# Kernel tuning notes

Hardware: AMD Instinct MI355X
Metric: run time of the kernel (lower is better)

## Reference

```python
import jax, jax.numpy as jnp
import numpy as np

# Model dims (eval mode: dropout off, no gate noise, no KV cache, start_pos=0)
B, T, C = 2, 2048, 1024
H, KV = 16, 4
HD = C // H            # 64
E, K = 8, 2            # n_experts, active_experts
FE, FS = 1024, 2048    # expert_inter_dim, shared inter_dim
EPS = 1e-6
BASE = 10000.0


def setup_inputs() -> dict:
    key = jax.random.key(0)
    ks = jax.random.split(key, 15)
    s = 0.02
    f32 = jnp.float32
    return {
        'x': jax.random.normal(ks[0], (B, T, C), f32),
        'norm1_w': jnp.ones((C,), f32),
        'norm2_w': jnp.ones((C,), f32),
        'wq': jax.random.normal(ks[1], (C, H * HD), f32) * s,
        'wk': jax.random.normal(ks[2], (C, KV * HD), f32) * s,
        'wv': jax.random.normal(ks[3], (C, KV * HD), f32) * s,
        'wo': jax.random.normal(ks[4], (H * HD, C), f32) * s,
        'gate_w': jax.random.normal(ks[5], (C, E), f32) * s,
        'exp_w1': jax.random.normal(ks[6], (E, C, FE), f32) * s,
        'exp_w2': jax.random.normal(ks[7], (E, C, FE), f32) * s,
        'exp_wp': jax.random.normal(ks[8], (E, FE, C), f32) * s,
        'sh_w1': jax.random.normal(ks[9], (C, FS), f32) * s,
        'sh_w2': jax.random.normal(ks[10], (C, FS), f32) * s,
        'sh_wp': jax.random.normal(ks[11], (FS, C), f32) * s,
    }


def _rms(x, w):
    return x * jax.lax.rsqrt(jnp.mean(x * x, -1, keepdims=True) + EPS) * w


def _rope_table(t, hd):
    freqs = 1.0 / (BASE ** (jnp.arange(0, hd, 2, dtype=jnp.float32) / hd))
    ang = jnp.outer(jnp.arange(t, dtype=jnp.float32), freqs)  # (T, hd/2)
    return jnp.stack([jnp.cos(ang), jnp.sin(ang)], -1)        # (T, hd/2, 2)


def _apply_rope(x, fc):
    # x: (B, T, nH, hd); fc: (T, hd/2, 2)
    xr = x.reshape(*x.shape[:-1], -1, 2)
    cos = fc[None, :, None, :, 0]
    sin = fc[None, :, None, :, 1]
    out = jnp.stack([xr[..., 0] * cos - xr[..., 1] * sin,
                     xr[..., 1] * cos + xr[..., 0] * sin], -1)
    return out.reshape(x.shape).astype(x.dtype)


def reference(x, norm1_w, norm2_w, wq, wk, wv, wo, gate_w,
              exp_w1, exp_w2, exp_wp, sh_w1, sh_w2, sh_wp):
    fc = _rope_table(T, HD)
    # --- GQA attention with RoPE ---
    h1 = _rms(x, norm1_w)
    q = (h1 @ wq).reshape(B, T, H, HD)
    k = (h1 @ wk).reshape(B, T, KV, HD)
    v = (h1 @ wv).reshape(B, T, KV, HD)
    q = _apply_rope(q, fc)
    k = _apply_rope(k, fc)
    rep = H // KV
    k = jnp.repeat(k, rep, axis=2)  # (B,T,H,HD)
    v = jnp.repeat(v, rep, axis=2)
    scores = jnp.einsum('bqhd,bkhd->bhqk', q, k) / jnp.sqrt(jnp.float32(HD))
    mask = jnp.where(jnp.tril(jnp.ones((T, T), bool)), 0.0, -1e9).astype(scores.dtype)
    att = jax.nn.softmax(scores + mask, axis=-1)
    o = jnp.einsum('bhqk,bkhd->bqhd', att, v).reshape(B, T, C) @ wo
    x1 = x + o
    # --- MoE block (top-k gate, dense masked combine == gather/scatter math) ---
    h2 = _rms(x1, norm2_w).reshape(-1, C)  # (N, C), N = B*T
    gate_logits = h2 @ gate_w              # (N, E)
    p = jax.nn.softmax(gate_logits, axis=-1)
    topw, topi = jax.lax.top_k(p, K)       # values == gather(p, indices)
    comb = jnp.sum(jax.nn.one_hot(topi, E, dtype=p.dtype) * topw[..., None], axis=1)  # (N, E)
    he = jax.nn.silu(jnp.einsum('nc,ecf->enf', h2, exp_w1)) * jnp.einsum('nc,ecf->enf', h2, exp_w2)
    ye = jnp.einsum('enf,efc->enc', he, exp_wp)
    y = jnp.einsum('enc,ne->nc', ye, comb)
    z = (jax.nn.silu(h2 @ sh_w1) * (h2 @ sh_w2)) @ sh_wp
    out = x1 + (y + z).reshape(B, T, C)
    return out, gate_logits
```

## Files before the change

kernel.cpp:

```cpp
#include <hip/hip_runtime.h>
#include <hip/hip_bf16.h>

#define TB 2
#define TT 2048
#define TC 1024
#define TH 16
#define TKV 4
#define THD 64
#define TE 8
#define TFE 1024
#define TFS 2048
#define NTOK 4096
#define NSLOT 8192

typedef __attribute__((ext_vector_type(4))) float f32x4;
typedef __attribute__((ext_vector_type(16))) float f32x16;
typedef __attribute__((ext_vector_type(8))) short s16x8;

__device__ __forceinline__ float bf2f(short s) {
    unsigned int u = ((unsigned int)(unsigned short)s) << 16;
    return __builtin_bit_cast(float, u);
}
__device__ __forceinline__ short f2bf(float f) {
    unsigned int u = __builtin_bit_cast(unsigned int, f);
    u = u + 0x7fffu + ((u >> 16) & 1u);
    return (short)(u >> 16);
}
__device__ __forceinline__ unsigned int cvtpk_bf16(float lo, float hi) {
    unsigned int r;
    asm volatile("v_cvt_pk_bf16_f32 %0, %1, %2" : "=v"(r) : "v"(lo), "v"(hi));
    return r;
}

__device__ __forceinline__ void gl_lds16(const void* g, void* l) {
    __builtin_amdgcn_global_load_lds((const __attribute__((address_space(1))) void*)g,
                                     (__attribute__((address_space(3))) void*)l,
                                     16, 0, 0);
}

__global__ __launch_bounds__(256) void k_transp(const float* __restrict__ in,
                                                short* __restrict__ out,
                                                int R, int Cd,
                                                size_t bs_in, size_t bs_out) {
    __shared__ float tile[32][33];
    const float* ip = in + bs_in * blockIdx.z;
    short* op = out + bs_out * blockIdx.z;
    int tx = threadIdx.x & 31, ty = threadIdx.x >> 5;
    int r0 = blockIdx.y * 32, c0 = blockIdx.x * 32;
    #pragma unroll
    for (int r = ty; r < 32; r += 8)
        tile[r][tx] = ip[(size_t)(r0 + r) * Cd + c0 + tx];
    __syncthreads();
    #pragma unroll
    for (int r = ty; r < 32; r += 8)
        op[(size_t)(c0 + r) * R + r0 + tx] = f2bf(tile[tx][r]);
}

__global__ __launch_bounds__(256) void k_transp_v(const short* __restrict__ qkv,
                                                  short* __restrict__ v_t) {
    __shared__ short tile[32][33];
    int z = blockIdx.z;
    int b = z >> 2, kvh = z & 3;
    const short* ip = qkv + (size_t)b * TT * 1536 + 1280 + kvh * 64;
    short* op = v_t + (size_t)z * THD * TT;
    int tx = threadIdx.x & 31, ty = threadIdx.x >> 5;
    int t0 = blockIdx.y * 32, d0 = blockIdx.x * 32;
    #pragma unroll
    for (int r = ty; r < 32; r += 8)
        tile[r][tx] = ip[(size_t)(t0 + r) * 1536 + d0 + tx];
    __syncthreads();
    #pragma unroll
    for (int r = ty; r < 32; r += 8)
        op[(size_t)(d0 + r) * TT + t0 + tx] = tile[tx][r];
}

__global__ void k_rope_table(float* __restrict__ rope) {
    int idx = blockIdx.x * 256 + threadIdx.x;
    if (idx >= TT * 32) return;
    int t = idx >> 5, i = idx & 31;
    float freq = expf(-(float)i * (1.0f / 32.0f) * 9.210340371976184f);
    float ang = (float)t * freq;
    rope[idx * 2 + 0] = cosf(ang);
    rope[idx * 2 + 1] = sinf(ang);
}

__global__ __launch_bounds__(256) void k_rmsnorm(const float* __restrict__ x,
                                                 const float* __restrict__ w,
                                                 short* __restrict__ out) {
    int row = blockIdx.x, t = threadIdx.x;
    float4 v = ((const float4*)(x + (size_t)row * TC))[t];
    float ss = v.x * v.x + v.y * v.y + v.z * v.z + v.w * v.w;
    #pragma unroll
    for (int off = 32; off; off >>= 1) ss += __shfl_xor(ss, off);
    __shared__ float red[4];
    if ((t & 63) == 0) red[t >> 6] = ss;
    __syncthreads();
    float rs = rsqrtf((red[0] + red[1] + red[2] + red[3]) * (1.0f / 1024.0f) + 1e-6f);
    float4 wv = ((const float4*)w)[t];
    short4 o;
    o.x = f2bf(v.x * rs * wv.x);
    o.y = f2bf(v.y * rs * wv.y);
    o.z = f2bf(v.z * rs * wv.z);
    o.w = f2bf(v.w * rs * wv.w);
    ((short4*)(out + (size_t)row * TC))[t] = o;
}

template <int EPI>
__global__ __launch_bounds__(256) void k_gemm128(const short* __restrict__ A,
                                                 const short* __restrict__ Bt,
                                                 void* __restrict__ outp,
                                                 const float* __restrict__ resid,
                                                 int M, int N, int K) {
    __shared__ short As0[128 * 32], As1[128 * 32];
    __shared__ short Bs0[128 * 32], Bs1[128 * 32];
    int tid = threadIdx.x;
    int brow = blockIdx.y * 128, bcol = blockIdx.x * 128;
    int wid = tid >> 6, lane = tid & 63;
    int wr = wid >> 1, wc = wid & 1, g = lane >> 4, c = lane & 15;
    int srow = wid * 32 + (lane >> 2);
    int scol = (lane & 3) * 8;
    const short* Ag0 = A + (size_t)(brow + srow) * K + scol;
    const short* Ag1 = A + (size_t)(brow + srow + 16) * K + scol;
    const short* Bg0 = Bt + (size_t)(bcol + srow) * K + scol;
    const short* Bg1 = Bt + (size_t)(bcol + srow + 16) * K + scol;
    int loff = __builtin_amdgcn_readfirstlane(wid * 2048);
    f32x4 acc[4][4] = {};

    gl_lds16(Ag0, (char*)As0 + loff);
    gl_lds16(Ag1, (char*)As0 + loff + 1024);
    gl_lds16(Bg0, (char*)Bs0 + loff);
    gl_lds16(Bg1, (char*)Bs0 + loff + 1024);
    __syncthreads();

    short* Ac = As0; short* Bc = Bs0;
    short* Aa = As1; short* Ba = Bs1;
    for (int kk = 0; kk < K; kk += 32) {
        int kn = kk + 32;
        if (kn < K) {
            gl_lds16(Ag0 + kn, (char*)Aa + loff);
            gl_lds16(Ag1 + kn, (char*)Aa + loff + 1024);
            gl_lds16(Bg0 + kn, (char*)Ba + loff);
            gl_lds16(Bg1 + kn, (char*)Ba + loff + 1024);
        }
        s16x8 af[4], bf[4];
        #pragma unroll
        for (int m = 0; m < 4; m++) af[m] = *(const s16x8*)(Ac + (wr * 64 + m * 16 + c) * 32 + g * 8);
        #pragma unroll
        for (int n = 0; n < 4; n++) bf[n] = *(const s16x8*)(Bc + (wc * 64 + n * 16 + c) * 32 + g * 8);
        #pragma unroll
        for (int m = 0; m < 4; m++)
            #pragma unroll
            for (int n = 0; n < 4; n++)
                acc[m][n] = __builtin_amdgcn_mfma_f32_16x16x32_bf16(af[m], bf[n], acc[m][n], 0, 0, 0);
        __syncthreads();
        short* t;
        t = Ac; Ac = Aa; Aa = t;
        t = Bc; Bc = Ba; Ba = t;
    }
    #pragma unroll
    for (int m = 0; m < 4; m++)
        #pragma unroll
        for (int n = 0; n < 4; n++)
            #pragma unroll
            for (int j = 0; j < 4; j++) {
                int row = brow + wr * 64 + m * 16 + g * 4 + j;
                int col = bcol + wc * 64 + n * 16 + c;
                float v = acc[m][n][j];
                if (EPI == 0)
                    ((short*)outp)[(size_t)row * N + col] = f2bf(v);
                else
                    ((float*)outp)[(size_t)row * N + col] = v + resid[(size_t)row * N + col];
            }
}

template <int EPI>
__global__ __launch_bounds__(256) void k_gemm64(const short* __restrict__ A,
                                                const short* __restrict__ Bt,
                                                void* __restrict__ outp,
                                                const float* __restrict__ resid,
                                                int M, int N, int K) {
    __shared__ short As0[128 * 32], As1[128 * 32];
    __shared__ short Bs0[64 * 32], Bs1[64 * 32];
    int tid = threadIdx.x;
    int brow = blockIdx.y * 128, bcol = blockIdx.x * 64;
    int wid = tid >> 6, lane = tid & 63;
    int wr = wid >> 1, wc = wid & 1, g = lane >> 4, c = lane & 15;
    int srow = wid * 32 + (lane >> 2);
    int scol = (lane & 3) * 8;
    const short* Ag0 = A + (size_t)(brow + srow) * K + scol;
    const short* Ag1 = A + (size_t)(brow + srow + 16) * K + scol;
    int sbrow = wid * 16 + (lane >> 2);
    const short* Bg = Bt + (size_t)(bcol + sbrow) * K + scol;
    int loffA = __builtin_amdgcn_readfirstlane(wid * 2048);
    int loffB = __builtin_amdgcn_readfirstlane(wid * 1024);
    f32x4 acc[4][2] = {};

    gl_lds16(Ag0, (char*)As0 + loffA);
    gl_lds16(Ag1, (char*)As0 + loffA + 1024);
    gl_lds16(Bg, (char*)Bs0 + loffB);
    __syncthreads();

    short* Ac = As0; short* Bc = Bs0;
    short* Aa = As1; short* Ba = Bs1;
    for (int kk = 0; kk < K; kk += 32) {
        int kn = kk + 32;
        if (kn < K) {
            gl_lds16(Ag0 + kn, (char*)Aa + loffA);
            gl_lds16(Ag1 + kn, (char*)Aa + loffA + 1024);
            gl_lds16(Bg + kn, (char*)Ba + loffB);
        }
        s16x8 af[4], bf[2];
        #pragma unroll
        for (int m = 0; m < 4; m++) af[m] = *(const s16x8*)(Ac + (wr * 64 + m * 16 + c) * 32 + g * 8);
        #pragma unroll
        for (int n = 0; n < 2; n++) bf[n] = *(const s16x8*)(Bc + (wc * 32 + n * 16 + c) * 32 + g * 8);
        #pragma unroll
        for (int m = 0; m < 4; m++)
            #pragma unroll
            for (int n = 0; n < 2; n++)
                acc[m][n] = __builtin_amdgcn_mfma_f32_16x16x32_bf16(af[m], bf[n], acc[m][n], 0, 0, 0);
        __syncthreads();
        short* t;
        t = Ac; Ac = Aa; Aa = t;
        t = Bc; Bc = Ba; Ba = t;
    }
    #pragma unroll
    for (int m = 0; m < 4; m++)
        #pragma unroll
        for (int n = 0; n < 2; n++)
            #pragma unroll
            for (int j = 0; j < 4; j++) {
                int row = brow + wr * 64 + m * 16 + g * 4 + j;
                int col = bcol + wc * 32 + n * 16 + c;
                float v = acc[m][n][j];
                if (EPI == 0)
                    ((short*)outp)[(size_t)row * N + col] = f2bf(v);
                else
                    ((float*)outp)[(size_t)row * N + col] = v + resid[(size_t)row * N + col];
            }
}

__global__ void k_rope_apply(const short* __restrict__ qkv,
                             const float* __restrict__ rope,
                             short* __restrict__ q_r,
                             short* __restrict__ k_r) {
    int idx = blockIdx.x * 256 + threadIdx.x;
    if (idx >= NTOK * 640) return;
    int row = idx / 640;
    int p = idx - row * 640;
    int b = row >> 11, t = row & 2047;
    const short* src = qkv + (size_t)row * 1536;
    if (p < 512) {
        int h = p >> 5, i = p & 31;
        float x0 = bf2f(src[h * 64 + 2 * i]);
        float x1 = bf2f(src[h * 64 + 2 * i + 1]);
        float cs = rope[(t * 32 + i) * 2], sn = rope[(t * 32 + i) * 2 + 1];
        size_t o = ((size_t)(b * TH + h) * TT + t) * THD + 2 * i;
        q_r[o]     = f2bf(x0 * cs - x1 * sn);
        q_r[o + 1] = f2bf(x1 * cs + x0 * sn);
    } else {
        int pk = p - 512;
        int kv = pk >> 5, i = pk & 31;
        float x0 = bf2f(src[1024 + kv * 64 + 2 * i]);
        float x1 = bf2f(src[1024 + kv * 64 + 2 * i + 1]);
        float cs = rope[(t * 32 + i) * 2], sn = rope[(t * 32 + i) * 2 + 1];
        size_t o = ((size_t)(b * TKV + kv) * TT + t) * THD + 2 * i;
        k_r[o]     = f2bf(x0 * cs - x1 * sn);
        k_r[o + 1] = f2bf(x1 * cs + x0 * sn);
    }
}

__global__ __launch_bounds__(256) void k_attn(const short* __restrict__ q_r,
                                              const short* __restrict__ k_r,
                                              const short* __restrict__ v_t,
                                              short* __restrict__ attn_o) {
    int w = threadIdx.x >> 6, lane = threadIdx.x & 63;
    int qt = 63 - (blockIdx.x * 4 + w);
    int qbase = qt * 32;
    int bh = blockIdx.y;
    int b = bh >> 4, h = bh & 15, kv = h >> 2;
    int q32 = lane & 31, hi = lane >> 5;

    const short* qp = q_r + ((size_t)(b * TH + h) * TT + qbase) * THD;
    const short* kp = k_r + ((size_t)(b * TKV + kv) * TT) * THD;
    const short* vp = v_t + ((size_t)(b * TKV + kv) * THD) * TT;

    s16x8 qf[4];
    #pragma unroll
    for (int dc = 0; dc < 4; dc++)
        qf[dc] = *(const s16x8*)(qp + q32 * THD + dc * 16 + hi * 8);

    f32x16 ot0 = {}, ot1 = {};
    float mrun = -1e30f, lrun = 0.f;
    int nkt = (qbase + 95) >> 6;

    for (int kt = 0; kt < nkt; kt++) {
        int ktb = kt * 64;
        f32x16 st0 = {}, st1 = {};
        s16x8 kf0[4], kf1[4];
        #pragma unroll
        for (int dc = 0; dc < 4; dc++) {
            kf0[dc] = *(const s16x8*)(kp + (size_t)(ktb + q32) * THD + dc * 16 + hi * 8);
            kf1[dc] = *(const s16x8*)(kp + (size_t)(ktb + 32 + q32) * THD + dc * 16 + hi * 8);
        }
        s16x8 vf[8];
        #pragma unroll
        for (int dt = 0; dt < 2; dt++)
            #pragma unroll
            for (int kc = 0; kc < 4; kc++)
                vf[dt * 4 + kc] = *(const s16x8*)(vp + (size_t)(dt * 32 + q32) * TT + ktb + kc * 16 + hi * 8);

        __builtin_amdgcn_s_setprio(1);
        #pragma unroll
        for (int dc = 0; dc < 4; dc++) {
            st0 = __builtin_amdgcn_mfma_f32_32x32x16_bf16(kf0[dc], qf[dc], st0, 0, 0, 0);
            st1 = __builtin_amdgcn_mfma_f32_32x32x16_bf16(kf1[dc], qf[dc], st1, 0, 0, 0);
        }
        __builtin_amdgcn_s_setprio(0);

        bool domask = (kt == nkt - 1);
        int qabs = qbase + q32;
        #pragma unroll
        for (int r = 0; r < 16; r++) {
            int kploc = (r & 3) + 8 * (r >> 2) + 4 * hi;
            float s0 = st0[r] * 0.125f;
            float s1 = st1[r] * 0.125f;
            if (domask) {
                if (ktb + kploc > qabs) s0 = -1e30f;
                if (ktb + 32 + kploc > qabs) s1 = -1e30f;
            }
            st0[r] = s0; st1[r] = s1;
        }
        float pm = st0[0];
        #pragma unroll
        for (int r = 1; r < 16; r++) pm = fmaxf(pm, st0[r]);
        #pragma unroll
        for (int r = 0; r < 16; r++) pm = fmaxf(pm, st1[r]);
        pm = fmaxf(pm, __shfl_xor(pm, 32));
        float mnew = fmaxf(mrun, pm);
        float al = __expf(mrun - mnew);
        mrun = mnew;
        float rs = 0.f;
        #pragma unroll
        for (int r = 0; r < 16; r++) {
            float e0 = __expf(st0[r] - mnew); st0[r] = e0; rs += e0;
            float e1 = __expf(st1[r] - mnew); st1[r] = e1; rs += e1;
        }
        rs += __shfl_xor(rs, 32);
        lrun = lrun * al + rs;
        #pragma unroll
        for (int r = 0; r < 16; r++) { ot0[r] *= al; ot1[r] *= al; }

        unsigned int w0[8], w1[8];
        #pragma unroll
        for (int j = 0; j < 8; j++) {
            w0[j] = cvtpk_bf16(st0[2 * j], st0[2 * j + 1]);
            w1[j] = cvtpk_bf16(st1[2 * j], st1[2 * j + 1]);
        }
        s16x8 pf[4];
        #pragma unroll
        for (int kc = 0; kc < 4; kc++) {
            unsigned int* ww = (kc < 2) ? w0 : w1;
            int kcl = kc & 1;
            unsigned int x0 = ww[4 * kcl + 0], y0 = ww[4 * kcl + 2];
            unsigned int x1 = ww[4 * kcl + 1], y1 = ww[4 * kcl + 3];
            asm volatile("v_permlane32_swap_b32 %0, %1" : "+v"(x0), "+v"(y0));
            asm volatile("v_permlane32_swap_b32 %0, %1" : "+v"(x1), "+v"(y1));
            unsigned int fr[4] = {x0, x1, y0, y1};
            pf[kc] = __builtin_bit_cast(s16x8, *(ulong2*)fr);
        }
        __builtin_amdgcn_s_setprio(1);
        #pragma unroll
        for (int kc = 0; kc < 4; kc++) {
            ot0 = __builtin_amdgcn_mfma_f32_32x32x16_bf16(vf[kc], pf[kc], ot0, 0, 0, 0);
            ot1 = __builtin_amdgcn_mfma_f32_32x32x16_bf16(vf[4 + kc], pf[kc], ot1, 0, 0, 0);
        }
        __builtin_amdgcn_s_setprio(0);
    }
    float inv = 1.0f / lrun;
    short* orow = attn_o + (size_t)(b * TT + qbase + q32) * TC + h * THD;
    #pragma unroll
    for (int s = 0; s < 4; s++) {
        short4 v0, v1;
        v0.x = f2bf(ot0[4 * s + 0] * inv); v0.y = f2bf(ot0[4 * s + 1] * inv);
        v0.z = f2bf(ot0[4 * s + 2] * inv); v0.w = f2bf(ot0[4 * s + 3] * inv);
        v1.x = f2bf(ot1[4 * s + 0] * inv); v1.y = f2bf(ot1[4 * s + 1] * inv);
        v1.z = f2bf(ot1[4 * s + 2] * inv); v1.w = f2bf(ot1[4 * s + 3] * inv);
        *(short4*)(orow + 8 * s + 4 * hi) = v0;
        *(short4*)(orow + 32 + 8 * s + 4 * hi) = v1;
    }
}

__global__ __launch_bounds__(256) void k_gate(const float* __restrict__ x1,
                                              const float* __restrict__ n2w,
                                              const float* __restrict__ gate_w,
                                              float* __restrict__ gl,
                                              int* __restrict__ cnt,
                                              int* __restrict__ te,
                                              int* __restrict__ tls,
                                              float* __restrict__ tw) {
    int w = threadIdx.x >> 6, lane = threadIdx.x & 63;
    int n = blockIdx.x * 4 + w;
    const float* xp = x1 + (size_t)n * TC;
    float ss = 0.f;
    for (int i = lane; i < TC; i += 64) { float v = xp[i]; ss += v * v; }
    #pragma unroll
    for (int off = 32; off; off >>= 1) ss += __shfl_xor(ss, off);
    float rs = rsqrtf(ss * (1.0f / 1024.0f) + 1e-6f);
    int e = lane & 7, ch = lane >> 3;
    float acc = 0.f;
    for (int i = 0; i < 128; i++) {
        int cc = ch * 128 + i;
        acc += xp[cc] * rs * n2w[cc] * gate_w[(size_t)cc * TE + e];
    }
    acc += __shfl_xor(acc, 8);
    acc += __shfl_xor(acc, 16);
    acc += __shfl_xor(acc, 32);
    float logit = acc;
    if (lane < 8) gl[(size_t)n * TE + lane] = logit;
    float mx = logit;
    mx = fmaxf(mx, __shfl_xor(mx, 1)); mx = fmaxf(mx, __shfl_xor(mx, 2)); mx = fmaxf(mx, __shfl_xor(mx, 4));
    float ex = __expf(logit - mx);
    float sm = ex;
    sm += __shfl_xor(sm, 1); sm += __shfl_xor(sm, 2); sm += __shfl_xor(sm, 4);
    float pp = ex / sm;
    float m1 = pp;
    m1 = fmaxf(m1, __shfl_xor(m1, 1)); m1 = fmaxf(m1, __shfl_xor(m1, 2)); m1 = fmaxf(m1, __shfl_xor(m1, 4));
    int cand = (pp == m1) ? e : 8;
    int e0 = cand;
    e0 = min(e0, __shfl_xor(e0, 1)); e0 = min(e0, __shfl_xor(e0, 2)); e0 = min(e0, __shfl_xor(e0, 4));
    float p2 = (e == e0) ? -1.0f : pp;
    float m2 = p2;
    m2 = fmaxf(m2, __shfl_xor(m2, 1)); m2 = fmaxf(m2, __shfl_xor(m2, 2)); m2 = fmaxf(m2, __shfl_xor(m2, 4));
    int cand2 = (p2 == m2) ? e : 8;
    int e1 = cand2;
    e1 = min(e1, __shfl_xor(e1, 1)); e1 = min(e1, __shfl_xor(e1, 2)); e1 = min(e1, __shfl_xor(e1, 4));
    if (lane == 0) {
        int ls0 = atomicAdd(&cnt[e0], 1);
        int ls1 = atomicAdd(&cnt[e1], 1);
        te[n * 2] = e0; te[n * 2 + 1] = e1;
        tls[n * 2] = ls0; tls[n * 2 + 1] = ls1;
        tw[n * 2] = m1; tw[n * 2 + 1] = m2;
    }
}

__global__ void k_prefix(const int* __restrict__ cnt, int* __restrict__ basep) {
    if (threadIdx.x == 0) {
        int s = 0;
        for (int e = 0; e < TE; e++) { basep[e] = s; s += cnt[e]; }
    }
}

__global__ void k_scatter(const int* __restrict__ te, const int* __restrict__ tls,
                          const float* __restrict__ tw, const int* __restrict__ basep,
                          int* __restrict__ tlist, float* __restrict__ slotw,
                          int* __restrict__ sot) {
    int n = blockIdx.x * 256 + threadIdx.x;
    if (n >= NTOK) return;
    int s0 = basep[te[n * 2]] + tls[n * 2];
    int s1 = basep[te[n * 2 + 1]] + tls[n * 2 + 1];
    tlist[s0] = n; tlist[s1] = n;
    slotw[s0] = tw[n * 2]; slotw[s1] = tw[n * 2 + 1];
    sot[n * 2] = s0; sot[n * 2 + 1] = s1;
}

__global__ __launch_bounds__(512) void k_ffn(const short* __restrict__ A,
                                             const short* __restrict__ eB1,
                                             const short* __restrict__ eB2,
                                             const short* __restrict__ sB1,
                                             const short* __restrict__ sB2,
                                             short* __restrict__ he,
                                             short* __restrict__ shm,
                                             const int* __restrict__ cnt,
                                             const int* __restrict__ basep,
                                             const int* __restrict__ tlist,
                                             const float* __restrict__ slotw) {
    int z = blockIdx.z;
    int moe = (z < 8);
    int nt = blockIdx.x, mt = blockIdx.y;
    int ce = 0, base = 0;
    if (moe) {
        if (nt >= 8) return;
        ce = cnt[z];
        if (mt * 128 >= ce) return;
        base = basep[z];
    }
    __shared__ short As0[128 * 32], As1[128 * 32];
    __shared__ short B1s0[128 * 32], B1s1[128 * 32];
    __shared__ short B2s0[128 * 32], B2s1[128 * 32];
    int tid = threadIdx.x, wid = tid >> 6, lane = tid & 63;
    int wr = wid >> 2, wc = wid & 3, g = lane >> 4, c = lane & 15;
    const int K = TC;
    int srow = wid * 16 + (lane >> 2);
    int scol = (lane & 3) * 8;
    size_t arow;
    if (moe) {
        int l0 = mt * 128 + srow; if (l0 >= ce) l0 = ce - 1;
        arow = (size_t)tlist[base + l0];
    } else {
        arow = (size_t)(mt * 128 + srow);
    }
    const short* Ag = A + arow * (size_t)K + scol;
    const short* B1g;
    const short* B2g;
    if (moe) {
        B1g = eB1 + ((size_t)z * TFE + (size_t)(nt * 128 + srow)) * K + scol;
        B2g = eB2 + ((size_t)z * TFE + (size_t)(nt * 128 + srow)) * K + scol;
    } else {
        B1g = sB1 + (size_t)(nt * 128 + srow) * K + scol;
        B2g = sB2 + (size_t)(nt * 128 + srow) * K + scol;
    }
    int loff = __builtin_amdgcn_readfirstlane(wid * 1024);
    f32x4 a1[4][2] = {}, a2[4][2] = {};

    gl_lds16(Ag, (char*)As0 + loff);
    gl_lds16(B1g, (char*)B1s0 + loff);
    gl_lds16(B2g, (char*)B2s0 + loff);
    __syncthreads();

    short* Ac = As0;  short* B1c = B1s0;  short* B2c = B2s0;
    short* Aa = As1;  short* B1a = B1s1;  short* B2a = B2s1;
    for (int kk = 0; kk < K; kk += 32) {
        int kn = kk + 32;
        if (kn < K) {
            gl_lds16(Ag + kn, (char*)Aa + loff);
            gl_lds16(B1g + kn, (char*)B1a + loff);
            gl_lds16(B2g + kn, (char*)B2a + loff);
        }
        s16x8 af[4], b1[2], b2[2];
        #pragma unroll
        for (int m_ = 0; m_ < 4; m_++) af[m_] = *(const s16x8*)(Ac + (wr * 64 + m_ * 16 + c) * 32 + g * 8);
        #pragma unroll
        for (int n = 0; n < 2; n++) {
            b1[n] = *(const s16x8*)(B1c + (wc * 32 + n * 16 + c) * 32 + g * 8);
            b2[n] = *(const s16x8*)(B2c + (wc * 32 + n * 16 + c) * 32 + g * 8);
        }
        #pragma unroll
        for (int m_ = 0; m_ < 4; m_++)
            #pragma unroll
            for (int n = 0; n < 2; n++) {
                a1[m_][n] = __builtin_amdgcn_mfma_f32_16x16x32_bf16(af[m_], b1[n], a1[m_][n], 0, 0, 0);
                a2[m_][n] = __builtin_amdgcn_mfma_f32_16x16x32_bf16(af[m_], b2[n], a2[m_][n], 0, 0, 0);
            }
        __syncthreads();
        short* t;
        t = Ac; Ac = Aa; Aa = t;
        t = B1c; B1c = B1a; B1a = t;
        t = B2c; B2c = B2a; B2a = t;
    }
    #pragma unroll
    for (int m_ = 0; m_ < 4; m_++)
        #pragma unroll
        for (int n = 0; n < 2; n++)
            #pragma unroll
            for (int j = 0; j < 4; j++) {
                int lrow = mt * 128 + wr * 64 + m_ * 16 + g * 4 + j;
                if (moe && lrow >= ce) continue;
                int col = nt * 128 + wc * 32 + n * 16 + c;
                float g1 = a1[m_][n][j], g2 = a2[m_][n][j];
                float v = g1 / (1.0f + __expf(-g1)) * g2;
                if (moe) {
                    v *= slotw[base + lrow];
                    he[(size_t)(base + lrow) * TFE + col] = f2bf(v);
                } else {
                    shm[(size_t)lrow * TFS + col] = f2bf(v);
                }
            }
}

__global__ __launch_bounds__(256) void k_moe2(const short* __restrict__ he,
                                              const short* __restrict__ Wpt,
                                              short* __restrict__ ye,
                                              const int* __restrict__ cnt,
                                              const int* __restrict__ basep) {
    int e = blockIdx.z;
    int ce = cnt[e];
    int mt = blockIdx.y;
    if (mt * 128 >= ce) return;
    int base = basep[e];
    int nt = blockIdx.x;
    __shared__ short As0[128 * 32], As1[128 * 32];
    __shared__ short Bs0[128 * 32], Bs1[128 * 32];
    int tid = threadIdx.x, wid = tid >> 6, lane = tid & 63;
    int wr = wid >> 1, wc = wid & 1, g = lane >> 4, c = lane & 15;
    int srow = wid * 32 + (lane >> 2);
    int scol = (lane & 3) * 8;
    const short* Ag0 = he + (size_t)(base + mt * 128 + srow) * TFE + scol;
    const short* Ag1 = Ag0 + (size_t)16 * TFE;
    const short* Bg0 = Wpt + ((size_t)e * 1024 + nt * 128 + srow) * TFE + scol;
    const short* Bg1 = Bg0 + (size_t)16 * TFE;
    int loff = __builtin_amdgcn_readfirstlane(wid * 2048);
    f32x4 acc[4][4] = {};

    gl_lds16(Ag0, (char*)As0 + loff);
    gl_lds16(Ag1, (char*)As0 + loff + 1024);
    gl_lds16(Bg0, (char*)Bs0 + loff);
    gl_lds16(Bg1, (char*)Bs0 + loff + 1024);
    __syncthreads();

    short* Ac = As0; short* Bc = Bs0;
    short* Aa = As1; short* Ba = Bs1;
    for (int kk = 0; kk < TFE; kk += 32) {
        int kn = kk + 32;
        if (kn < TFE) {
            gl_lds16(Ag0 + kn, (char*)Aa + loff);
            gl_lds16(Ag1 + kn, (char*)Aa + loff + 1024);
            gl_lds16(Bg0 + kn, (char*)Ba + loff);
            gl_lds16(Bg1 + kn, (char*)Ba + loff + 1024);
        }
        s16x8 af[4], bf[4];
        #pragma unroll
        for (int m = 0; m < 4; m++) af[m] = *(const s16x8*)(Ac + (wr * 64 + m * 16 + c) * 32 + g * 8);
        #pragma unroll
        for (int n = 0; n < 4; n++) bf[n] = *(const s16x8*)(Bc + (wc * 64 + n * 16 + c) * 32 + g * 8);
        #pragma unroll
        for (int m = 0; m < 4; m++)
            #pragma unroll
            for (int n = 0; n < 4; n++)
                acc[m][n] = __builtin_amdgcn_mfma_f32_16x16x32_bf16(af[m], bf[n], acc[m][n], 0, 0, 0);
        __syncthreads();
        short* t;
        t = Ac; Ac = Aa; Aa = t;
        t = Bc; Bc = Ba; Ba = t;
    }
    #pragma unroll
    for (int m = 0; m < 4; m++)
        #pragma unroll
        for (int n = 0; n < 4; n++)
            #pragma unroll
            for (int j = 0; j < 4; j++) {
                int lrow = mt * 128 + wr * 64 + m * 16 + g * 4 + j;
                if (lrow >= ce) continue;
                int col = nt * 128 + wc * 64 + n * 16 + c;
                ye[(size_t)(base + lrow) * TC + col] = f2bf(acc[m][n][j]);
            }
}

__global__ __launch_bounds__(256) void k_final(const short* __restrict__ A,
                                               const short* __restrict__ Bt,
                                               const float* __restrict__ x1,
                                               const short* __restrict__ ye,
                                               const int* __restrict__ sot,
                                               float* __restrict__ outp) {
    __shared__ short As0[128 * 32], As1[128 * 32];
    __shared__ short Bs0[64 * 32], Bs1[64 * 32];
    const int K = TFS;
    int tid = threadIdx.x;
    int brow = blockIdx.y * 128, bcol = blockIdx.x * 64;
    int wid = tid >> 6, lane = tid & 63;
    int wr = wid >> 1, wc = wid & 1, g = lane >> 4, c = lane & 15;
    int srow = wid * 32 + (lane >> 2);
    int scol = (lane & 3) * 8;
    const short* Ag0 = A + (size_t)(brow + srow) * K + scol;
    const short* Ag1 = A + (size_t)(brow + srow + 16) * K + scol;
    int sbrow = wid * 16 + (lane >> 2);
    const short* Bg = Bt + (size_t)(bcol + sbrow) * K + scol;
    int loffA = __builtin_amdgcn_readfirstlane(wid * 2048);
    int loffB = __builtin_amdgcn_readfirstlane(wid * 1024);
    f32x4 acc[4][2] = {};

    gl_lds16(Ag0, (char*)As0 + loffA);
    gl_lds16(Ag1, (char*)As0 + loffA + 1024);
    gl_lds16(Bg, (char*)Bs0 + loffB);
    __syncthreads();

    short* Ac = As0; short* Bc = Bs0;
    short* Aa = As1; short* Ba = Bs1;
    for (int kk = 0; kk < K; kk += 32) {
        int kn = kk + 32;
        if (kn < K) {
            gl_lds16(Ag0 + kn, (char*)Aa + loffA);
            gl_lds16(Ag1 + kn, (char*)Aa + loffA + 1024);
            gl_lds16(Bg + kn, (char*)Ba + loffB);
        }
        s16x8 af[4], bf[2];
        #pragma unroll
        for (int m = 0; m < 4; m++) af[m] = *(const s16x8*)(Ac + (wr * 64 + m * 16 + c) * 32 + g * 8);
        #pragma unroll
        for (int n = 0; n < 2; n++) bf[n] = *(const s16x8*)(Bc + (wc * 32 + n * 16 + c) * 32 + g * 8);
        #pragma unroll
        for (int m = 0; m < 4; m++)
            #pragma unroll
            for (int n = 0; n < 2; n++)
                acc[m][n] = __builtin_amdgcn_mfma_f32_16x16x32_bf16(af[m], bf[n], acc[m][n], 0, 0, 0);
        __syncthreads();
        short* t;
        t = Ac; Ac = Aa; Aa = t;
        t = Bc; Bc = Ba; Ba = t;
    }
    #pragma unroll
    for (int m = 0; m < 4; m++)
        #pragma unroll
        for (int n = 0; n < 2; n++)
            #pragma unroll
            for (int j = 0; j < 4; j++) {
                int row = brow + wr * 64 + m * 16 + g * 4 + j;
                int col = bcol + wc * 32 + n * 16 + c;
                int s0 = sot[row * 2], s1 = sot[row * 2 + 1];
                float v = acc[m][n][j] + x1[(size_t)row * TC + col]
                        + bf2f(ye[(size_t)s0 * TC + col]) + bf2f(ye[(size_t)s1 * TC + col]);
                outp[(size_t)row * TC + col] = v;
            }
}

extern "C" void kernel_launch(void* const* d_in, const int* in_sizes, int n_in,
                              void* d_out, int out_size, void* d_ws, size_t ws_size,
                              hipStream_t stream) {
    const float* x     = (const float*)d_in[0];
    const float* n1w   = (const float*)d_in[1];
    const float* n2w   = (const float*)d_in[2];
    const float* wq    = (const float*)d_in[3];
    const float* wk    = (const float*)d_in[4];
    const float* wv    = (const float*)d_in[5];
    const float* wo    = (const float*)d_in[6];
    const float* gatew = (const float*)d_in[7];
    const float* ew1   = (const float*)d_in[8];
    const float* ew2   = (const float*)d_in[9];
    const float* ewp   = (const float*)d_in[10];
    const float* sw1   = (const float*)d_in[11];
    const float* sw2   = (const float*)d_in[12];
    const float* swp   = (const float*)d_in[13];
    float* outp = (float*)d_out;

    char* p = (char*)d_ws;
    auto alloc = [&](size_t bytes) -> char* {
        char* r = p;
        p += (bytes + 255) & ~(size_t)255;
        return r;
    };
    short* wqkv_t = (short*)alloc(1536 * 1024 * 2);
    short* wo_t   = (short*)alloc(1024 * 1024 * 2);
    short* ew1_t  = (short*)alloc((size_t)8 * 1024 * 1024 * 2);
    short* ew2_t  = (short*)alloc((size_t)8 * 1024 * 1024 * 2);
    short* ewp_t  = (short*)alloc((size_t)8 * 1024 * 1024 * 2);
    short* sw1_t  = (short*)alloc((size_t)2048 * 1024 * 2);
    short* sw2_t  = (short*)alloc((size_t)2048 * 1024 * 2);
    short* swp_t  = (short*)alloc((size_t)1024 * 2048 * 2);
    short* h1     = (short*)alloc((size_t)NTOK * 1024 * 2);
    short* qkv    = (short*)alloc((size_t)NTOK * 1536 * 2);
    short* q_r    = (short*)alloc((size_t)TB * TH * TT * THD * 2);
    short* k_r    = (short*)alloc((size_t)TB * TKV * TT * THD * 2);
    short* v_t    = (short*)alloc((size_t)TB * TKV * THD * TT * 2);
    short* attn_o = (short*)alloc((size_t)NTOK * 1024 * 2);
    float* x1     = (float*)alloc((size_t)NTOK * 1024 * 4);
    short* h2     = (short*)alloc((size_t)NTOK * 1024 * 2);
    float* rope   = (float*)alloc((size_t)TT * 32 * 2 * 4);
    int*   cnt    = (int*)alloc(256);
    int*   basep  = (int*)alloc(256);
    int*   te     = (int*)alloc((size_t)NTOK * 2 * 4);
    int*   tls    = (int*)alloc((size_t)NTOK * 2 * 4);
    float* tw     = (float*)alloc((size_t)NTOK * 2 * 4);
    int*   tlist  = (int*)alloc((size_t)NSLOT * 4);
    float* slotw  = (float*)alloc((size_t)NSLOT * 4);
    int*   sot    = (int*)alloc((size_t)NTOK * 2 * 4);
    short* he     = (short*)alloc((size_t)NSLOT * TFE * 2);
    short* ye     = (short*)alloc((size_t)NSLOT * TC * 2);
    short* shm    = (short*)alloc((size_t)NTOK * TFS * 2);

    dim3 blk(256);

    k_transp<<<dim3(32, 32, 1), blk, 0, stream>>>(wq, wqkv_t, 1024, 1024, 0, 0);
    k_transp<<<dim3(8, 32, 1), blk, 0, stream>>>(wk, wqkv_t + 1024 * 1024, 1024, 256, 0, 0);
    k_transp<<<dim3(8, 32, 1), blk, 0, stream>>>(wv, wqkv_t + 1280 * 1024, 1024, 256, 0, 0);
    k_transp<<<dim3(32, 32, 1), blk, 0, stream>>>(wo, wo_t, 1024, 1024, 0, 0);
    k_transp<<<dim3(32, 32, 8), blk, 0, stream>>>(ew1, ew1_t, 1024, 1024, 1048576, 1048576);
    k_transp<<<dim3(32, 32, 8), blk, 0, stream>>>(ew2, ew2_t, 1024, 1024, 1048576, 1048576);
    k_transp<<<dim3(32, 32, 8), blk, 0, stream>>>(ewp, ewp_t, 1024, 1024, 1048576, 1048576);
    k_transp<<<dim3(64, 32, 1), blk, 0, stream>>>(sw1, sw1_t, 1024, 2048, 0, 0);
    k_transp<<<dim3(64, 32, 1), blk, 0, stream>>>(sw2, sw2_t, 1024, 2048, 0, 0);
    k_transp<<<dim3(32, 64, 1), blk, 0, stream>>>(swp, swp_t, 2048, 1024, 0, 0);

    k_rope_table<<<(TT * 32 + 255) / 256, blk, 0, stream>>>(rope);

    k_rmsnorm<<<NTOK, blk, 0, stream>>>(x, n1w, h1);
    k_gemm128<0><<<dim3(12, 32), blk, 0, stream>>>(h1, wqkv_t, qkv, nullptr, NTOK, 1536, 1024);
    k_rope_apply<<<(NTOK * 640 + 255) / 256, blk, 0, stream>>>(qkv, rope, q_r, k_r);
    k_transp_v<<<dim3(2, 64, 8), blk, 0, stream>>>(qkv, v_t);

    k_attn<<<dim3(16, TB * TH), blk, 0, stream>>>(q_r, k_r, v_t, attn_o);

    k_gemm64<1><<<dim3(16, 32), blk, 0, stream>>>(attn_o, wo_t, x1, x, NTOK, 1024, 1024);

    k_rmsnorm<<<NTOK, blk, 0, stream>>>(x1, n2w, h2);

    hipMemsetAsync(cnt, 0, 64, stream);
    k_gate<<<NTOK / 4, blk, 0, stream>>>(x1, n2w, gatew, outp + (size_t)NTOK * TC, cnt, te, tls, tw);
    k_prefix<<<1, 64, 0, stream>>>(cnt, basep);
    k_scatter<<<NTOK / 256, blk, 0, stream>>>(te, tls, tw, basep, tlist, slotw, sot);

    k_ffn<<<dim3(16, 32, 9), dim3(512), 0, stream>>>(h2, ew1_t, ew2_t, sw1_t, sw2_t, he, shm,
                                                     cnt, basep, tlist, slotw);
    k_moe2<<<dim3(8, 32, 8), blk, 0, stream>>>(he, ewp_t, ye, cnt, basep);

    k_final<<<dim3(16, 32), blk, 0, stream>>>(shm, swp_t, x1, ye, sot, outp);

    (void)in_sizes; (void)n_in; (void)out_size; (void)ws_size;
}
```

Baseline: 724.4 us.

## Restructure GEMM pipelines with explicit waits, vectorize RoPE, lazy-rescale attention softmax

Rewrites the main loops of all GEMM kernels (gemm128, gemm64, ffn, moe2, final). They now prefetch two stages ahead, replace __syncthreads with explicit vmcnt/lgkmcnt waits and raw barriers, and raise wave priority around the MFMA block. The RoPE kernel now handles 8 elements per thread with vector loads and stores. The attention softmax moves to exp2 with the log2e factor folded into the scale, and rescales the running max only when it grows past a threshold. Together these aim to cut barrier stalls and memory latency. They add risk from fragile manual waitcnt accounting in the reused buffers.

```diff
diff --git a/kernel.cpp b/kernel.cpp
--- a/kernel.cpp
+++ b/kernel.cpp
@@ -37,6 +37,9 @@
                                      (__attribute__((address_space(3))) void*)l,
                                      16, 0, 0);
 }
+
+#define WAIT_VM(N) asm volatile("s_waitcnt vmcnt(" #N ")" ::: "memory")
+#define WAIT_LGKM0() asm volatile("s_waitcnt lgkmcnt(0)" ::: "memory")
 
 __global__ __launch_bounds__(256) void k_transp(const float* __restrict__ in,
                                                 short* __restrict__ out,
@@ -125,37 +128,43 @@
     const short* Bg1 = Bt + (size_t)(bcol + srow + 16) * K + scol;
     int loff = __builtin_amdgcn_readfirstlane(wid * 2048);
     f32x4 acc[4][4] = {};
-
-    gl_lds16(Ag0, (char*)As0 + loff);
-    gl_lds16(Ag1, (char*)As0 + loff + 1024);
-    gl_lds16(Bg0, (char*)Bs0 + loff);
-    gl_lds16(Bg1, (char*)Bs0 + loff + 1024);
-    __syncthreads();
-
-    short* Ac = As0; short* Bc = Bs0;
-    short* Aa = As1; short* Ba = Bs1;
-    for (int kk = 0; kk < K; kk += 32) {
-        int kn = kk + 32;
-        if (kn < K) {
-            gl_lds16(Ag0 + kn, (char*)Aa + loff);
-            gl_lds16(Ag1 + kn, (char*)Aa + loff + 1024);
-            gl_lds16(Bg0 + kn, (char*)Ba + loff);
-            gl_lds16(Bg1 + kn, (char*)Ba + loff + 1024);
-        }
+    auto stage = [&](int kq, short* A_, short* B_) {
+        gl_lds16(Ag0 + kq, (char*)A_ + loff);
+        gl_lds16(Ag1 + kq, (char*)A_ + loff + 1024);
+        gl_lds16(Bg0 + kq, (char*)B_ + loff);
+        gl_lds16(Bg1 + kq, (char*)B_ + loff + 1024);
+    };
+    stage(0, As0, Bs0);
+    stage(32, As1, Bs1);
+    WAIT_VM(4);
+    __builtin_amdgcn_s_barrier();
+    const int T = K >> 5;
+    for (int t = 0; t < T; ++t) {
+        short* Ac = (t & 1) ? As1 : As0;
+        short* Bc = (t & 1) ? Bs1 : Bs0;
         s16x8 af[4], bf[4];
         #pragma unroll
         for (int m = 0; m < 4; m++) af[m] = *(const s16x8*)(Ac + (wr * 64 + m * 16 + c) * 32 + g * 8);
         #pragma unroll
         for (int n = 0; n < 4; n++) bf[n] = *(const s16x8*)(Bc + (wc * 64 + n * 16 + c) * 32 + g * 8);
+        WAIT_LGKM0();
+        __builtin_amdgcn_sched_barrier(0);
+        __builtin_amdgcn_s_barrier();
+        if (t + 2 < T) {
+            stage((t + 2) << 5, Ac, Bc);
+            WAIT_VM(4);
+        } else if (t + 1 < T) {
+            WAIT_VM(0);
+        }
+        __builtin_amdgcn_s_barrier();
+        __builtin_amdgcn_sched_barrier(0);
+        __builtin_amdgcn_s_setprio(1);
         #pragma unroll
         for (int m = 0; m < 4; m++)
             #pragma unroll
             for (int n = 0; n < 4; n++)
                 acc[m][n] = __builtin_amdgcn_mfma_f32_16x16x32_bf16(af[m], bf[n], acc[m][n], 0, 0, 0);
-        __syncthreads();
-        short* t;
-        t = Ac; Ac = Aa; Aa = t;
-        t = Bc; Bc = Ba; Ba = t;
+        __builtin_amdgcn_s_setprio(0);
     }
     #pragma unroll
     for (int m = 0; m < 4; m++)
@@ -194,35 +203,42 @@
     int loffA = __builtin_amdgcn_readfirstlane(wid * 2048);
     int loffB = __builtin_amdgcn_readfirstlane(wid * 1024);
     f32x4 acc[4][2] = {};
-
-    gl_lds16(Ag0, (char*)As0 + loffA);
-    gl_lds16(Ag1, (char*)As0 + loffA + 1024);
-    gl_lds16(Bg, (char*)Bs0 + loffB);
-    __syncthreads();
-
-    short* Ac = As0; short* Bc = Bs0;
-    short* Aa = As1; short* Ba = Bs1;
-    for (int kk = 0; kk < K; kk += 32) {
-        int kn = kk + 32;
-        if (kn < K) {
-            gl_lds16(Ag0 + kn, (char*)Aa + loffA);
-            gl_lds16(Ag1 + kn, (char*)Aa + loffA + 1024);
-            gl_lds16(Bg + kn, (char*)Ba + loffB);
-        }
+    auto stage = [&](int kq, short* A_, short* B_) {
+        gl_lds16(Ag0 + kq, (char*)A_ + loffA);
+        gl_lds16(Ag1 + kq, (char*)A_ + loffA + 1024);
+        gl_lds16(Bg + kq, (char*)B_ + loffB);
+    };
+    stage(0, As0, Bs0);
+    stage(32, As1, Bs1);
+    WAIT_VM(3);
+    __builtin_amdgcn_s_barrier();
+    const int T = K >> 5;
+    for (int t = 0; t < T; ++t) {
+        short* Ac = (t & 1) ? As1 : As0;
+        short* Bc = (t & 1) ? Bs1 : Bs0;
         s16x8 af[4], bf[2];
         #pragma unroll
         for (int m = 0; m < 4; m++) af[m] = *(const s16x8*)(Ac + (wr * 64 + m * 16 + c) * 32 + g * 8);
         #pragma unroll
         for (int n = 0; n < 2; n++) bf[n] = *(const s16x8*)(Bc + (wc * 32 + n * 16 + c) * 32 + g * 8);
+        WAIT_LGKM0();
+        __builtin_amdgcn_sched_barrier(0);
+        __builtin_amdgcn_s_barrier();
+        if (t + 2 < T) {
+            stage((t + 2) << 5, Ac, Bc);
+            WAIT_VM(3);
+        } else if (t + 1 < T) {
+            WAIT_VM(0);
+        }
+        __builtin_amdgcn_s_barrier();
+        __builtin_amdgcn_sched_barrier(0);
+        __builtin_amdgcn_s_setprio(1);
         #pragma unroll
         for (int m = 0; m < 4; m++)
             #pragma unroll
             for (int n = 0; n < 2; n++)
                 acc[m][n] = __builtin_amdgcn_mfma_f32_16x16x32_bf16(af[m], bf[n], acc[m][n], 0, 0, 0);
-        __syncthreads();
-        short* t;
-        t = Ac; Ac = Aa; Aa = t;
-        t = Bc; Bc = Ba; Ba = t;
+        __builtin_amdgcn_s_setprio(0);
     }
     #pragma unroll
     for (int m = 0; m < 4; m++)
@@ -245,29 +261,34 @@
                              short* __restrict__ q_r,
                              short* __restrict__ k_r) {
     int idx = blockIdx.x * 256 + threadIdx.x;
-    if (idx >= NTOK * 640) return;
-    int row = idx / 640;
-    int p = idx - row * 640;
+    if (idx >= NTOK * 160) return;
+    int row = idx / 160;
+    int p8 = idx - row * 160;
     int b = row >> 11, t = row & 2047;
     const short* src = qkv + (size_t)row * 1536;
-    if (p < 512) {
-        int h = p >> 5, i = p & 31;
-        float x0 = bf2f(src[h * 64 + 2 * i]);
-        float x1 = bf2f(src[h * 64 + 2 * i + 1]);
-        float cs = rope[(t * 32 + i) * 2], sn = rope[(t * 32 + i) * 2 + 1];
-        size_t o = ((size_t)(b * TH + h) * TT + t) * THD + 2 * i;
-        q_r[o]     = f2bf(x0 * cs - x1 * sn);
-        q_r[o + 1] = f2bf(x1 * cs + x0 * sn);
-    } else {
-        int pk = p - 512;
-        int kv = pk >> 5, i = pk & 31;
-        float x0 = bf2f(src[1024 + kv * 64 + 2 * i]);
-        float x1 = bf2f(src[1024 + kv * 64 + 2 * i + 1]);
-        float cs = rope[(t * 32 + i) * 2], sn = rope[(t * 32 + i) * 2 + 1];
-        size_t o = ((size_t)(b * TKV + kv) * TT + t) * THD + 2 * i;
-        k_r[o]     = f2bf(x0 * cs - x1 * sn);
-        k_r[o + 1] = f2bf(x1 * cs + x0 * sn);
-    }
+    bool isq = p8 < 128;
+    int pk = isq ? p8 : (p8 - 128);
+    int hh = pk >> 3;
+    int i0 = (pk & 7) * 8;
+    int srcoff = (isq ? 0 : 1024) + hh * 64 + i0;
+    s16x8 v = *(const s16x8*)(src + srcoff);
+    const float* rp = rope + ((size_t)t * 32 + (i0 >> 1)) * 2;
+    float4 r0 = *(const float4*)rp;
+    float4 r1 = *(const float4*)(rp + 4);
+    s16x8 ov;
+    float cc, ss, x0, x1;
+    cc = r0.x; ss = r0.y; x0 = bf2f(v[0]); x1 = bf2f(v[1]);
+    ov[0] = f2bf(x0 * cc - x1 * ss); ov[1] = f2bf(x1 * cc + x0 * ss);
+    cc = r0.z; ss = r0.w; x0 = bf2f(v[2]); x1 = bf2f(v[3]);
+    ov[2] = f2bf(x0 * cc - x1 * ss); ov[3] = f2bf(x1 * cc + x0 * ss);
+    cc = r1.x; ss = r1.y; x0 = bf2f(v[4]); x1 = bf2f(v[5]);
+    ov[4] = f2bf(x0 * cc - x1 * ss); ov[5] = f2bf(x1 * cc + x0 * ss);
+    cc = r1.z; ss = r1.w; x0 = bf2f(v[6]); x1 = bf2f(v[7]);
+    ov[6] = f2bf(x0 * cc - x1 * ss); ov[7] = f2bf(x1 * cc + x0 * ss);
+    if (isq)
+        *(s16x8*)(q_r + ((size_t)(b * TH + hh) * TT + t) * THD + i0) = ov;
+    else
+        *(s16x8*)(k_r + ((size_t)(b * TKV + hh) * TT + t) * THD + i0) = ov;
 }
 
 __global__ __launch_bounds__(256) void k_attn(const short* __restrict__ q_r,
@@ -293,6 +314,7 @@
     f32x16 ot0 = {}, ot1 = {};
     float mrun = -1e30f, lrun = 0.f;
     int nkt = (qbase + 95) >> 6;
+    const float SC = 0.125f * 1.44269504088896f;
 
     for (int kt = 0; kt < nkt; kt++) {
         int ktb = kt * 64;
@@ -323,8 +345,8 @@
         #pragma unroll
         for (int r = 0; r < 16; r++) {
             int kploc = (r & 3) + 8 * (r >> 2) + 4 * hi;
-            float s0 = st0[r] * 0.125f;
-            float s1 = st1[r] * 0.125f;
+            float s0 = st0[r] * SC;
+            float s1 = st1[r] * SC;
             if (domask) {
                 if (ktb + kploc > qabs) s0 = -1e30f;
                 if (ktb + 32 + kploc > qabs) s1 = -1e30f;
@@ -337,19 +359,22 @@
         #pragma unroll
         for (int r = 0; r < 16; r++) pm = fmaxf(pm, st1[r]);
         pm = fmaxf(pm, __shfl_xor(pm, 32));
-        float mnew = fmaxf(mrun, pm);
-        float al = __expf(mrun - mnew);
-        mrun = mnew;
+        if (__any(pm > mrun + 8.0f)) {
+            float mnew = fmaxf(mrun, pm);
+            float al = exp2f(mrun - mnew);
+            mrun = mnew;
+            lrun *= al;
+            #pragma unroll
+            for (int r = 0; r < 16; r++) { ot0[r] *= al; ot1[r] *= al; }
+        }
         float rs = 0.f;
         #pragma unroll
         for (int r = 0; r < 16; r++) {
-            float e0 = __expf(st0[r] - mnew); st0[r] = e0; rs += e0;
-            float e1 = __expf(st1[r] - mnew); st1[r] = e1; rs += e1;
+            float e0 = exp2f(st0[r] - mrun); st0[r] = e0; rs += e0;
+            float e1 = exp2f(st1[r] - mrun); st1[r] = e1; rs += e1;
         }
         rs += __shfl_xor(rs, 32);
-        lrun = lrun * al + rs;
-        #pragma unroll
-        for (int r = 0; r < 16; r++) { ot0[r] *= al; ot1[r] *= al; }
+        lrun += rs;
 
         unsigned int w0[8], w1[8];
         #pragma unroll
@@ -512,21 +537,20 @@
     }
     int loff = __builtin_amdgcn_readfirstlane(wid * 1024);
     f32x4 a1[4][2] = {}, a2[4][2] = {};
-
-    gl_lds16(Ag, (char*)As0 + loff);
-    gl_lds16(B1g, (char*)B1s0 + loff);
-    gl_lds16(B2g, (char*)B2s0 + loff);
-    __syncthreads();
-
-    short* Ac = As0;  short* B1c = B1s0;  short* B2c = B2s0;
-    short* Aa = As1;  short* B1a = B1s1;  short* B2a = B2s1;
-    for (int kk = 0; kk < K; kk += 32) {
-        int kn = kk + 32;
-        if (kn < K) {
-            gl_lds16(Ag + kn, (char*)Aa + loff);
-            gl_lds16(B1g + kn, (char*)B1a + loff);
-            gl_lds16(B2g + kn, (char*)B2a + loff);
-        }
+    auto stage = [&](int kq, short* A_, short* B1_, short* B2_) {
+        gl_lds16(Ag + kq, (char*)A_ + loff);
+        gl_lds16(B1g + kq, (char*)B1_ + loff);
+        gl_lds16(B2g + kq, (char*)B2_ + loff);
+    };
+    stage(0, As0, B1s0, B2s0);
+    stage(32, As1, B1s1, B2s1);
+    WAIT_VM(3);
+    __builtin_amdgcn_s_barrier();
+    const int T = K >> 5;
+    for (int t = 0; t < T; ++t) {
+        short* Ac = (t & 1) ? As1 : As0;
+        short* B1c = (t & 1) ? B1s1 : B1s0;
+        short* B2c = (t & 1) ? B2s1 : B2s0;
         s16x8 af[4], b1[2], b2[2];
         #pragma unroll
         for (int m_ = 0; m_ < 4; m_++) af[m_] = *(const s16x8*)(Ac + (wr * 64 + m_ * 16 + c) * 32 + g * 8);
@@ -535,6 +559,18 @@
             b1[n] = *(const s16x8*)(B1c + (wc * 32 + n * 16 + c) * 32 + g * 8);
             b2[n] = *(const s16x8*)(B2c + (wc * 32 + n * 16 + c) * 32 + g * 8);
         }
+        WAIT_LGKM0();
+        __builtin_amdgcn_sched_barrier(0);
+        __builtin_amdgcn_s_barrier();
+        if (t + 2 < T) {
+            stage((t + 2) << 5, Ac, B1c, B2c);
+            WAIT_VM(3);
+        } else if (t + 1 < T) {
+            WAIT_VM(0);
+        }
+        __builtin_amdgcn_s_barrier();
+        __builtin_amdgcn_sched_barrier(0);
+        __builtin_amdgcn_s_setprio(1);
         #pragma unroll
         for (int m_ = 0; m_ < 4; m_++)
             #pragma unroll
@@ -542,11 +578,7 @@
                 a1[m_][n] = __builtin_amdgcn_mfma_f32_16x16x32_bf16(af[m_], b1[n], a1[m_][n], 0, 0, 0);
                 a2[m_][n] = __builtin_amdgcn_mfma_f32_16x16x32_bf16(af[m_], b2[n], a2[m_][n], 0, 0, 0);
             }
-        __syncthreads();
-        short* t;
-        t = Ac; Ac = Aa; Aa = t;
-        t = B1c; B1c = B1a; B1a = t;
-        t = B2c; B2c = B2a; B2a = t;
+        __builtin_amdgcn_s_setprio(0);
     }
     #pragma unroll
     for (int m_ = 0; m_ < 4; m_++)
@@ -591,37 +623,43 @@
     const short* Bg1 = Bg0 + (size_t)16 * TFE;
     int loff = __builtin_amdgcn_readfirstlane(wid * 2048);
     f32x4 acc[4][4] = {};
-
-    gl_lds16(Ag0, (char*)As0 + loff);
-    gl_lds16(Ag1, (char*)As0 + loff + 1024);
-    gl_lds16(Bg0, (char*)Bs0 + loff);
-    gl_lds16(Bg1, (char*)Bs0 + loff + 1024);
-    __syncthreads();
-
-    short* Ac = As0; short* Bc = Bs0;
-    short* Aa = As1; short* Ba = Bs1;
-    for (int kk = 0; kk < TFE; kk += 32) {
-        int kn = kk + 32;
-        if (kn < TFE) {
-            gl_lds16(Ag0 + kn, (char*)Aa + loff);
-            gl_lds16(Ag1 + kn, (char*)Aa + loff + 1024);
-            gl_lds16(Bg0 + kn, (char*)Ba + loff);
-            gl_lds16(Bg1 + kn, (char*)Ba + loff + 1024);
-        }
+    auto stage = [&](int kq, short* A_, short* B_) {
+        gl_lds16(Ag0 + kq, (char*)A_ + loff);
+        gl_lds16(Ag1 + kq, (char*)A_ + loff + 1024);
+        gl_lds16(Bg0 + kq, (char*)B_ + loff);
+        gl_lds16(Bg1 + kq, (char*)B_ + loff + 1024);
+    };
+    stage(0, As0, Bs0);
+    stage(32, As1, Bs1);
+    WAIT_VM(4);
+    __builtin_amdgcn_s_barrier();
+    const int T = TFE >> 5;
+    for (int t = 0; t < T; ++t) {
+        short* Ac = (t & 1) ? As1 : As0;
+        short* Bc = (t & 1) ? Bs1 : Bs0;
         s16x8 af[4], bf[4];
         #pragma unroll
         for (int m = 0; m < 4; m++) af[m] = *(const s16x8*)(Ac + (wr * 64 + m * 16 + c) * 32 + g * 8);
         #pragma unroll
         for (int n = 0; n < 4; n++) bf[n] = *(const s16x8*)(Bc + (wc * 64 + n * 16 + c) * 32 + g * 8);
+        WAIT_LGKM0();
+        __builtin_amdgcn_sched_barrier(0);
+        __builtin_amdgcn_s_barrier();
+        if (t + 2 < T) {
+            stage((t + 2) << 5, Ac, Bc);
+            WAIT_VM(4);
+        } else if (t + 1 < T) {
+            WAIT_VM(0);
+        }
+        __builtin_amdgcn_s_barrier();
+        __builtin_amdgcn_sched_barrier(0);
+        __builtin_amdgcn_s_setprio(1);
         #pragma unroll
         for (int m = 0; m < 4; m++)
             #pragma unroll
             for (int n = 0; n < 4; n++)
                 acc[m][n] = __builtin_amdgcn_mfma_f32_16x16x32_bf16(af[m], bf[n], acc[m][n], 0, 0, 0);
-        __syncthreads();
-        short* t;
-        t = Ac; Ac = Aa; Aa = t;
-        t = Bc; Bc = Ba; Ba = t;
+        __builtin_amdgcn_s_setprio(0);
     }
     #pragma unroll
     for (int m = 0; m < 4; m++)
@@ -658,35 +696,42 @@
     int loffA = __builtin_amdgcn_readfirstlane(wid * 2048);
     int loffB = __builtin_amdgcn_readfirstlane(wid * 1024);
     f32x4 acc[4][2] = {};
-
-    gl_lds16(Ag0, (char*)As0 + loffA);
-    gl_lds16(Ag1, (char*)As0 + loffA + 1024);
-    gl_lds16(Bg, (char*)Bs0 + loffB);
-    __syncthreads();
-
-    short* Ac = As0; short* Bc = Bs0;
-    short* Aa = As1; short* Ba = Bs1;
-    for (int kk = 0; kk < K; kk += 32) {
-        int kn = kk + 32;
-        if (kn < K) {
-            gl_lds16(Ag0 + kn, (char*)Aa + loffA);
-            gl_lds16(Ag1 + kn, (char*)Aa + loffA + 1024);
-            gl_lds16(Bg + kn, (char*)Ba + loffB);
-        }
+    auto stage = [&](int kq, short* A_, short* B_) {
+        gl_lds16(Ag0 + kq, (char*)A_ + loffA);
+        gl_lds16(Ag1 + kq, (char*)A_ + loffA + 1024);
+        gl_lds16(Bg + kq, (char*)B_ + loffB);
+    };
+    stage(0, As0, Bs0);
+    stage(32, As1, Bs1);
+    WAIT_VM(3);
+    __builtin_amdgcn_s_barrier();
+    const int T = K >> 5;
+    for (int t = 0; t < T; ++t) {
+        short* Ac = (t & 1) ? As1 : As0;
+        short* Bc = (t & 1) ? Bs1 : Bs0;
         s16x8 af[4], bf[2];
         #pragma unroll
         for (int m = 0; m < 4; m++) af[m] = *(const s16x8*)(Ac + (wr * 64 + m * 16 + c) * 32 + g * 8);
         #pragma unroll
         for (int n = 0; n < 2; n++) bf[n] = *(const s16x8*)(Bc + (wc * 32 + n * 16 + c) * 32 + g * 8);
+        WAIT_LGKM0();
+        __builtin_amdgcn_sched_barrier(0);
+        __builtin_amdgcn_s_barrier();
+        if (t + 2 < T) {
+            stage((t + 2) << 5, Ac, Bc);
+            WAIT_VM(3);
+        } else if (t + 1 < T) {
+            WAIT_VM(0);
+        }
+        __builtin_amdgcn_s_barrier();
+        __builtin_amdgcn_sched_barrier(0);
+        __builtin_amdgcn_s_setprio(1);
         #pragma unroll
         for (int m = 0; m < 4; m++)
             #pragma unroll
             for (int n = 0; n < 2; n++)
                 acc[m][n] = __builtin_amdgcn_mfma_f32_16x16x32_bf16(af[m], bf[n], acc[m][n], 0, 0, 0);
-        __syncthreads();
-        short* t;
-        t = Ac; Ac = Aa; Aa = t;
-        t = Bc; Bc = Ba; Ba = t;
+        __builtin_amdgcn_s_setprio(0);
     }
     #pragma unroll
     for (int m = 0; m < 4; m++)
@@ -774,7 +819,7 @@
 
     k_rmsnorm<<<NTOK, blk, 0, stream>>>(x, n1w, h1);
     k_gemm128<0><<<dim3(12, 32), blk, 0, stream>>>(h1, wqkv_t, qkv, nullptr, NTOK, 1536, 1024);
-    k_rope_apply<<<(NTOK * 640 + 255) / 256, blk, 0, stream>>>(qkv, rope, q_r, k_r);
+    k_rope_apply<<<(NTOK * 160 + 255) / 256, blk, 0, stream>>>(qkv, rope, q_r, k_r);
     k_transp_v<<<dim3(2, 64, 8), blk, 0, stream>>>(qkv, v_t);
 
     k_attn<<<dim3(16, TB * TH), blk, 0, stream>>>(q_r, k_r, v_t, attn_o);
```

Measured after the change: 715.4 us. No clear change (-1.2%).
